# Performance work log

Hardware: AMD Instinct MI355X
Metric: run time of the kernel (lower is better)

The kernel has to match this reference:

```python
import jax, jax.numpy as jnp
import numpy as np

B, S, D = 4, 4096, 1024
DFF = 4 * D
ACTIVE = 1024  # ceil(S * 0.25)


def setup_inputs() -> dict:
    key = jax.random.key(0)
    ks = jax.random.split(key, 4)
    x = jax.random.normal(ks[0], (B, S, D), dtype=jnp.float32)
    rw = jax.random.normal(ks[1], (D,), dtype=jnp.float32) * 0.02
    rb = jnp.zeros((1,), dtype=jnp.float32)
    w1 = jax.random.normal(ks[2], (D, DFF), dtype=jnp.float32) * 0.02
    b1 = jnp.zeros((DFF,), dtype=jnp.float32)
    w2 = jax.random.normal(ks[3], (DFF, D), dtype=jnp.float32) * 0.02
    b2 = jnp.zeros((D,), dtype=jnp.float32)
    return {"x": x, "rw": rw, "rb": rb, "w1": w1, "b1": b1,
            "w2": w2, "b2": b2, "active_tokens": ACTIVE}


def reference(x, rw, rb, w1, b1, w2, b2, active_tokens):
    b, s, d = x.shape
    # router: Linear(n_embd, 1) -> [B, S] scores
    scores = jnp.einsum('bsd,d->bs', x, rw) + rb[0]
    # top-k tokens per batch row
    _, idx = jax.lax.top_k(scores, active_tokens)          # [B, K] int32
    sel = jnp.take_along_axis(x, idx[..., None], axis=1)   # [B, K, D]
    # dense MLP on selected tokens (exact GELU as in torch nn.GELU)
    h = jax.nn.gelu(jnp.einsum('bkd,df->bkf', sel, w1) + b1, approximate=False)
    out = jnp.einsum('bkf,fd->bkd', h, w2) + b2            # [B, K, D]
    # sigmoid gate from router scores of selected tokens
    gates = jax.nn.sigmoid(jnp.take_along_axis(scores, idx, axis=1))  # [B, K]
    out = out * gates[..., None]
    # scatter back into zeros at selected positions
    flat_idx = (idx + jnp.arange(b, dtype=idx.dtype)[:, None] * s).reshape(-1)
    flat_out = jnp.zeros((b * s, d), dtype=out.dtype)
    flat_out = flat_out.at[flat_idx].set(out.reshape(-1, d))
    return flat_out.reshape(b, s, d)
```

## Files before the change

kernel.cpp:

```cpp
#include <hip/hip_runtime.h>
#include <hip/hip_bf16.h>
#include <cstdint>
#include <cstddef>

#define Bz 4
#define Sz 4096
#define Dz 1024
#define DFFz 4096
#define KACT 1024

typedef __bf16 bf16;
typedef __attribute__((ext_vector_type(8))) __bf16 bf16x8;
typedef __attribute__((ext_vector_type(4))) __bf16 bf16x4;
typedef __attribute__((ext_vector_type(4))) float f32x4;

__device__ __forceinline__ void async16(const void* g, void* l) {
  __builtin_amdgcn_global_load_lds(
      (const __attribute__((address_space(1))) void*)g,
      (__attribute__((address_space(3))) void*)l, 16, 0, 0);
}

__global__ __launch_bounds__(256) void prep_k(const float* __restrict__ x,
                                              const float* __restrict__ rw,
                                              const float* __restrict__ rb,
                                              float* __restrict__ scores,
                                              float4* __restrict__ out4,
                                              const float* __restrict__ w1,
                                              bf16* __restrict__ w1T,
                                              const float* __restrict__ w2,
                                              bf16* __restrict__ w2T) {
  __shared__ float t[32][33];
  const int bid = blockIdx.x;
  const int tid = threadIdx.x;
  if (bid < 4096) {
    int row = bid * 4 + (tid >> 6);
    int lane = tid & 63;
    const float4* xr = (const float4*)(x + (size_t)row * Dz);
    const float4* wr = (const float4*)rw;
    float acc = 0.f;
#pragma unroll
    for (int i = 0; i < 4; ++i) {
      float4 a = xr[lane + i * 64];
      float4 w = wr[lane + i * 64];
      acc += a.x * w.x + a.y * w.y + a.z * w.z + a.w * w.w;
    }
#pragma unroll
    for (int d = 32; d; d >>= 1) acc += __shfl_down(acc, d, 64);
    if (lane == 0) scores[row] = acc + rb[0];
    float4* o = out4 + (size_t)bid * 4 * (Dz / 4);
    const float4 z = make_float4(0.f, 0.f, 0.f, 0.f);
#pragma unroll
    for (int i = 0; i < 4; ++i) o[tid + i * 256] = z;
  } else {
    const float* in; bf16* outp; int R, C, bx, by;
    if (bid < 8192) {
      in = w1; outp = w1T; R = Dz; C = DFFz;
      bx = (bid - 4096) & 127; by = (bid - 4096) >> 7;
    } else {
      in = w2; outp = w2T; R = DFFz; C = Dz;
      bx = (bid - 8192) & 31; by = (bid - 8192) >> 5;
    }
    int c0 = bx * 32, r0 = by * 32;
    int tx = tid & 31, ty = tid >> 5;
#pragma unroll
    for (int i = 0; i < 32; i += 8) t[ty + i][tx] = in[(size_t)(r0 + ty + i) * C + c0 + tx];
    __syncthreads();
#pragma unroll
    for (int i = 0; i < 32; i += 8)
      outp[(size_t)(c0 + ty + i) * R + r0 + tx] = (bf16)t[tx][ty + i];
  }
}

__global__ __launch_bounds__(256) void select_gather_k(
    const float* __restrict__ x, const float* __restrict__ scores,
    int* __restrict__ sel_idx, float* __restrict__ gates, bf16* __restrict__ Xsel) {
  int b = blockIdx.x >> 8;
  int s0 = (blockIdx.x & 255) * 16;
  __shared__ float sc[Sz];
  __shared__ int red[16][4];
  __shared__ int rk[16];
  const int tid = threadIdx.x;
  const int wave = tid >> 6, lane = tid & 63;
  const float* srow = scores + (size_t)b * Sz;
#pragma unroll
  for (int i = 0; i < 4; ++i)
    ((float4*)sc)[tid + i * 256] = ((const float4*)srow)[tid + i * 256];
  __syncthreads();
  float mine[16];
#pragma unroll
  for (int j = 0; j < 16; ++j) mine[j] = sc[s0 + j];
  int cnt[16] = {};
  for (int t = tid; t < Sz; t += 256) {
    float o = sc[t];
#pragma unroll
    for (int j = 0; j < 16; ++j)
      cnt[j] += (o > mine[j]) || (o == mine[j] && t < s0 + j);
  }
#pragma unroll
  for (int j = 0; j < 16; ++j) {
    int c = cnt[j];
#pragma unroll
    for (int d = 32; d; d >>= 1) c += __shfl_down(c, d, 64);
    if (lane == 0) red[j][wave] = c;
  }
  __syncthreads();
  if (tid < 16) {
    int rank = red[tid][0] + red[tid][1] + red[tid][2] + red[tid][3];
    rk[tid] = rank;
    if (rank < KACT) {
      int m = b * KACT + rank;
      sel_idx[m] = s0 + tid;
      gates[m] = 1.f / (1.f + expf(-sc[s0 + tid]));
    }
  }
  __syncthreads();
#pragma unroll
  for (int j = 0; j < 16; ++j) {
    int rank = rk[j];
    if (rank >= KACT) continue;
    int m = b * KACT + rank;
    float4 v = ((const float4*)(x + ((size_t)b * Sz + s0 + j) * Dz))[tid];
    bf16x4 o = {(bf16)v.x, (bf16)v.y, (bf16)v.z, (bf16)v.w};
    ((bf16x4*)(Xsel + (size_t)m * Dz))[tid] = o;
  }
}

#define STAGE128(k0)                                                           \
  {                                                                            \
    async16(Ag + (k0), &As[tid * 8]);                                          \
    async16(Ag + (size_t)64 * K + (k0), &As[2048 + tid * 8]);                  \
    async16(Bg + (k0), &Bs[tid * 8]);                                          \
    async16(Bg + (size_t)64 * K + (k0), &Bs[2048 + tid * 8]);                  \
  }

#define GEMM128_BODY(KV, KOFF, NITER)                                          \
  __shared__ __align__(16) bf16 As[128 * 32];                        \
  __shared__ __align__(16) bf16 Bs[128 * 32];                        \
  constexpr int K = (KV);                                                      \
  const int tid = threadIdx.x;                                                 \
  const int wave = tid >> 6, lane = tid & 63;                                  \
  const int quad = lane >> 4, l16 = lane & 15;                                 \
  const int m0 = blockIdx.y * 128, n0 = blockIdx.x * 128;                      \
  const int wm = (wave >> 1) * 64, wn = (wave & 1) * 64;                       \
    \
   \
  const bf16* Ag = A + (size_t)(m0 + (tid >> 2)) * K + (KOFF) + (tid & 3) * 8; \
  const bf16* Bg = Bt + (size_t)(n0 + (tid >> 2)) * K + (KOFF) + (tid & 3) * 8;\
  f32x4 acc[4][4] = {};                                                        \
  STAGE128(0)                                                                  \
  for (int it = 0; it < (NITER); ++it) {                                       \
    __syncthreads();                 \
    bf16x8 af[4], bfr[4];                                                      \
    _Pragma("unroll")                                                          \
    for (int i = 0; i < 4; ++i) {                                              \
      af[i] = *(const bf16x8*)&As[(wm + i * 16 + l16) * 32 + quad * 8];        \
      bfr[i] = *(const bf16x8*)&Bs[(wn + i * 16 + l16) * 32 + quad * 8];       \
    }                                                                          \
    _Pragma("unroll")                                                          \
    for (int mi = 0; mi < 4; ++mi)                                             \
      _Pragma("unroll")                                                        \
      for (int ni = 0; ni < 4; ++ni)                                           \
        acc[mi][ni] = __builtin_amdgcn_mfma_f32_16x16x32_bf16(af[mi], bfr[ni], acc[mi][ni], 0, 0, 0); \
    __syncthreads();              \
    if (it + 1 < (NITER)) { STAGE128((it + 1) * 32) }                          \
  }

__global__ __launch_bounds__(256) void gemm1_k(const bf16* __restrict__ A,
                                               const bf16* __restrict__ Bt,
                                               const float* __restrict__ bias,
                                               bf16* __restrict__ H) {
  GEMM128_BODY(Dz, 0, Dz / 32)
#pragma unroll
  for (int mi = 0; mi < 4; ++mi) {
    int mbase = m0 + wm + mi * 16 + quad * 4;
#pragma unroll
    for (int ni = 0; ni < 4; ++ni) {
      int n = n0 + wn + ni * 16 + l16;
      float bn = bias[n];
#pragma unroll
      for (int r = 0; r < 4; ++r) {
        float z = acc[mi][ni][r] + bn;
        float g = 0.5f * z * (1.f + erff(z * 0.70710678118654752f));
        H[(size_t)(mbase + r) * DFFz + n] = (bf16)g;
      }
    }
  }
}

__global__ __launch_bounds__(256) void gemm2_k(const bf16* __restrict__ A,
                                               const bf16* __restrict__ Bt,
                                               bf16* __restrict__ P) {
  GEMM128_BODY(DFFz, blockIdx.z * 2048, 2048 / 32)
  bf16* Pc = P + (size_t)blockIdx.z * Bz * KACT * Dz;
#pragma unroll
  for (int mi = 0; mi < 4; ++mi) {
    int mbase = m0 + wm + mi * 16 + quad * 4;
#pragma unroll
    for (int ni = 0; ni < 4; ++ni) {
      int n = n0 + wn + ni * 16 + l16;
#pragma unroll
      for (int r = 0; r < 4; ++r)
        Pc[(size_t)(mbase + r) * Dz + n] = (bf16)acc[mi][ni][r];
    }
  }
}

__global__ __launch_bounds__(256) void reduce_k(const bf16* __restrict__ P,
                                                const float* __restrict__ bias,
                                                const int* __restrict__ sel_idx,
                                                const float* __restrict__ gates,
                                                float* __restrict__ out) {
  int m = blockIdx.x;
  int b = m >> 10;
  int s = sel_idx[m];
  float gt = gates[m];
  int tid = threadIdx.x;
  const bf16x4* p0 = (const bf16x4*)(P + (size_t)m * Dz);
  const bf16x4* p1 = (const bf16x4*)(P + (size_t)Bz * KACT * Dz + (size_t)m * Dz);
  const float4* bv = (const float4*)bias;
  float4* orow = (float4*)(out + ((size_t)b * Sz + s) * Dz);
  bf16x4 a = p0[tid], c = p1[tid];
  float4 bb = bv[tid];
  float4 o;
  o.x = ((float)a[0] + (float)c[0] + bb.x) * gt;
  o.y = ((float)a[1] + (float)c[1] + bb.y) * gt;
  o.z = ((float)a[2] + (float)c[2] + bb.z) * gt;
  o.w = ((float)a[3] + (float)c[3] + bb.w) * gt;
  orow[tid] = o;
}

extern "C" void kernel_launch(void* const* d_in, const int* in_sizes, int n_in,
                              void* d_out, int out_size, void* d_ws, size_t ws_size,
                              hipStream_t stream) {
  (void)in_sizes; (void)n_in; (void)out_size; (void)ws_size;
  const float* x  = (const float*)d_in[0];
  const float* rw = (const float*)d_in[1];
  const float* rb = (const float*)d_in[2];
  const float* w1 = (const float*)d_in[3];
  const float* b1 = (const float*)d_in[4];
  const float* w2 = (const float*)d_in[5];
  const float* b2 = (const float*)d_in[6];
  float* out = (float*)d_out;

  char* ws = (char*)d_ws;
  float* scores = (float*)ws;  ws += (size_t)Bz * Sz * 4;
  int*   sel_idx = (int*)ws;   ws += (size_t)Bz * KACT * 4;
  float* gates = (float*)ws;   ws += (size_t)Bz * KACT * 4;
  bf16*  w2T = (bf16*)ws;      ws += (size_t)Dz * DFFz * 2;
  bf16*  H = (bf16*)ws;        ws += (size_t)Bz * KACT * DFFz * 2;
  bf16*  w1T = (bf16*)ws;      ws += (size_t)DFFz * Dz * 2;
  bf16*  Xsel = (bf16*)ws;     ws += (size_t)Bz * KACT * Dz * 2;
  bf16*  P = w1T;

  prep_k<<<3 * 4096, 256, 0, stream>>>(x, rw, rb, scores, (float4*)out, w1, w1T, w2, w2T);
  select_gather_k<<<Bz * (Sz / 16), 256, 0, stream>>>(x, scores, sel_idx, gates, Xsel);
  gemm1_k<<<dim3(DFFz / 128, (Bz * KACT) / 128), 256, 0, stream>>>(Xsel, w1T, b1, H);
  gemm2_k<<<dim3(Dz / 128, (Bz * KACT) / 128, 2), 256, 0, stream>>>(H, w2T, P);
  reduce_k<<<Bz * KACT, 256, 0, stream>>>(P, b2, sel_idx, gates, out);
}
```

Baseline: 300.9 us.

## Double-buffer GEMM tiles, swizzle blocks, fuse split-K reduce into gemm2 epilogue

Both GEMMs now use double-buffered LDS so async loads for the next K-slice are issued before the MFMAs on the current one, with one barrier per iteration instead of two. Block indices are swizzled for L2 locality, and MFMA sections are wrapped in s_setprio. Gemm2 drops split-K and uses a 128x64 tile over the full K range, writing bias-added, gated fp32 results straight into the scattered output rows. This removes the reduce kernel and the bf16 partial round-trip, at the cost of longer per-block K loops and uncoalesced-ish scatter stores from the MFMA layout.

```diff
diff --git a/kernel.cpp b/kernel.cpp
--- a/kernel.cpp
+++ b/kernel.cpp
@@ -125,51 +125,54 @@
   }
 }
 
-#define STAGE128(k0)                                                           \
-  {                                                                            \
-    async16(Ag + (k0), &As[tid * 8]);                                          \
-    async16(Ag + (size_t)64 * K + (k0), &As[2048 + tid * 8]);                  \
-    async16(Bg + (k0), &Bs[tid * 8]);                                          \
-    async16(Bg + (size_t)64 * K + (k0), &Bs[2048 + tid * 8]);                  \
-  }
-
-#define GEMM128_BODY(KV, KOFF, NITER)                                          \
-  __shared__ __align__(16) bf16 As[128 * 32];                        \
-  __shared__ __align__(16) bf16 Bs[128 * 32];                        \
-  constexpr int K = (KV);                                                      \
-  const int tid = threadIdx.x;                                                 \
-  const int wave = tid >> 6, lane = tid & 63;                                  \
-  const int quad = lane >> 4, l16 = lane & 15;                                 \
-  const int m0 = blockIdx.y * 128, n0 = blockIdx.x * 128;                      \
-  const int wm = (wave >> 1) * 64, wn = (wave & 1) * 64;                       \
-    \
-   \
-  const bf16* Ag = A + (size_t)(m0 + (tid >> 2)) * K + (KOFF) + (tid & 3) * 8; \
-  const bf16* Bg = Bt + (size_t)(n0 + (tid >> 2)) * K + (KOFF) + (tid & 3) * 8;\
-  f32x4 acc[4][4] = {};                                                        \
-  STAGE128(0)                                                                  \
-  for (int it = 0; it < (NITER); ++it) {                                       \
-    __syncthreads();                 \
-    bf16x8 af[4], bfr[4];                                                      \
-    _Pragma("unroll")                                                          \
-    for (int i = 0; i < 4; ++i) {                                              \
-      af[i] = *(const bf16x8*)&As[(wm + i * 16 + l16) * 32 + quad * 8];        \
-      bfr[i] = *(const bf16x8*)&Bs[(wn + i * 16 + l16) * 32 + quad * 8];       \
-    }                                                                          \
-    _Pragma("unroll")                                                          \
-    for (int mi = 0; mi < 4; ++mi)                                             \
-      _Pragma("unroll")                                                        \
-      for (int ni = 0; ni < 4; ++ni)                                           \
-        acc[mi][ni] = __builtin_amdgcn_mfma_f32_16x16x32_bf16(af[mi], bfr[ni], acc[mi][ni], 0, 0, 0); \
-    __syncthreads();              \
-    if (it + 1 < (NITER)) { STAGE128((it + 1) * 32) }                          \
-  }
 
 __global__ __launch_bounds__(256) void gemm1_k(const bf16* __restrict__ A,
                                                const bf16* __restrict__ Bt,
                                                const float* __restrict__ bias,
                                                bf16* __restrict__ H) {
-  GEMM128_BODY(Dz, 0, Dz / 32)
+  __shared__ __align__(16) bf16 As[2][128 * 32];
+  __shared__ __align__(16) bf16 Bs[2][128 * 32];
+  constexpr int K = Dz;
+  constexpr int NITER = Dz / 32;
+  const int tid = threadIdx.x;
+  const int wave = tid >> 6, lane = tid & 63;
+  const int quad = lane >> 4, l16 = lane & 15;
+  const int orig = blockIdx.y * 32 + blockIdx.x;
+  const int swz = ((orig & 7) << 7) | (orig >> 3);
+  const int m0 = (swz >> 5) * 128, n0 = (swz & 31) * 128;
+  const int wm = (wave >> 1) * 64, wn = (wave & 1) * 64;
+  const bf16* Ag = A + (size_t)(m0 + (tid >> 2)) * K + (tid & 3) * 8;
+  const bf16* Bg = Bt + (size_t)(n0 + (tid >> 2)) * K + (tid & 3) * 8;
+  f32x4 acc[4][4] = {};
+  async16(Ag, &As[0][tid * 8]);
+  async16(Ag + (size_t)64 * K, &As[0][2048 + tid * 8]);
+  async16(Bg, &Bs[0][tid * 8]);
+  async16(Bg + (size_t)64 * K, &Bs[0][2048 + tid * 8]);
+  __syncthreads();
+  for (int t = 0; t < NITER; ++t) {
+    const int cur = t & 1;
+    if (t + 1 < NITER) {
+      const int k0 = (t + 1) * 32;
+      async16(Ag + k0, &As[cur ^ 1][tid * 8]);
+      async16(Ag + (size_t)64 * K + k0, &As[cur ^ 1][2048 + tid * 8]);
+      async16(Bg + k0, &Bs[cur ^ 1][tid * 8]);
+      async16(Bg + (size_t)64 * K + k0, &Bs[cur ^ 1][2048 + tid * 8]);
+    }
+    bf16x8 af[4], bfr[4];
+#pragma unroll
+    for (int i = 0; i < 4; ++i) {
+      af[i] = *(const bf16x8*)&As[cur][(wm + i * 16 + l16) * 32 + quad * 8];
+      bfr[i] = *(const bf16x8*)&Bs[cur][(wn + i * 16 + l16) * 32 + quad * 8];
+    }
+    __builtin_amdgcn_s_setprio(1);
+#pragma unroll
+    for (int mi = 0; mi < 4; ++mi)
+#pragma unroll
+      for (int ni = 0; ni < 4; ++ni)
+        acc[mi][ni] = __builtin_amdgcn_mfma_f32_16x16x32_bf16(af[mi], bfr[ni], acc[mi][ni], 0, 0, 0);
+    __builtin_amdgcn_s_setprio(0);
+    __syncthreads();
+  }
 #pragma unroll
   for (int mi = 0; mi < 4; ++mi) {
     int mbase = m0 + wm + mi * 16 + quad * 4;
@@ -189,44 +192,68 @@
 
 __global__ __launch_bounds__(256) void gemm2_k(const bf16* __restrict__ A,
                                                const bf16* __restrict__ Bt,
-                                               bf16* __restrict__ P) {
-  GEMM128_BODY(DFFz, blockIdx.z * 2048, 2048 / 32)
-  bf16* Pc = P + (size_t)blockIdx.z * Bz * KACT * Dz;
+                                               const float* __restrict__ b2,
+                                               const int* __restrict__ sel_idx,
+                                               const float* __restrict__ gates,
+                                               float* __restrict__ out) {
+  __shared__ __align__(16) bf16 As[2][128 * 32];
+  __shared__ __align__(16) bf16 Bs[2][64 * 32];
+  constexpr int K = DFFz;
+  constexpr int NITER = DFFz / 32;
+  const int tid = threadIdx.x;
+  const int wave = tid >> 6, lane = tid & 63;
+  const int quad = lane >> 4, l16 = lane & 15;
+  const int orig = blockIdx.y * 16 + blockIdx.x;
+  const int swz = ((orig & 7) << 6) | (orig >> 3);
+  const int m0 = (swz >> 4) * 128, n0 = (swz & 15) * 64;
+  const int wm = (wave >> 1) * 64, wn = (wave & 1) * 32;
+  const bf16* Ag = A + (size_t)(m0 + (tid >> 2)) * K + (tid & 3) * 8;
+  const bf16* Bg = Bt + (size_t)(n0 + (tid >> 2)) * K + (tid & 3) * 8;
+  f32x4 acc[4][2] = {};
+  async16(Ag, &As[0][tid * 8]);
+  async16(Ag + (size_t)64 * K, &As[0][2048 + tid * 8]);
+  async16(Bg, &Bs[0][tid * 8]);
+  __syncthreads();
+  for (int t = 0; t < NITER; ++t) {
+    const int cur = t & 1;
+    if (t + 1 < NITER) {
+      const int k0 = (t + 1) * 32;
+      async16(Ag + k0, &As[cur ^ 1][tid * 8]);
+      async16(Ag + (size_t)64 * K + k0, &As[cur ^ 1][2048 + tid * 8]);
+      async16(Bg + k0, &Bs[cur ^ 1][tid * 8]);
+    }
+    bf16x8 af[4], bfr[2];
+#pragma unroll
+    for (int i = 0; i < 4; ++i)
+      af[i] = *(const bf16x8*)&As[cur][(wm + i * 16 + l16) * 32 + quad * 8];
+#pragma unroll
+    for (int i = 0; i < 2; ++i)
+      bfr[i] = *(const bf16x8*)&Bs[cur][(wn + i * 16 + l16) * 32 + quad * 8];
+    __builtin_amdgcn_s_setprio(1);
+#pragma unroll
+    for (int mi = 0; mi < 4; ++mi)
+#pragma unroll
+      for (int ni = 0; ni < 2; ++ni)
+        acc[mi][ni] = __builtin_amdgcn_mfma_f32_16x16x32_bf16(af[mi], bfr[ni], acc[mi][ni], 0, 0, 0);
+    __builtin_amdgcn_s_setprio(0);
+    __syncthreads();
+  }
 #pragma unroll
   for (int mi = 0; mi < 4; ++mi) {
-    int mbase = m0 + wm + mi * 16 + quad * 4;
-#pragma unroll
-    for (int ni = 0; ni < 4; ++ni) {
-      int n = n0 + wn + ni * 16 + l16;
-#pragma unroll
-      for (int r = 0; r < 4; ++r)
-        Pc[(size_t)(mbase + r) * Dz + n] = (bf16)acc[mi][ni][r];
-    }
-  }
-}
-
-__global__ __launch_bounds__(256) void reduce_k(const bf16* __restrict__ P,
-                                                const float* __restrict__ bias,
-                                                const int* __restrict__ sel_idx,
-                                                const float* __restrict__ gates,
-                                                float* __restrict__ out) {
-  int m = blockIdx.x;
-  int b = m >> 10;
-  int s = sel_idx[m];
-  float gt = gates[m];
-  int tid = threadIdx.x;
-  const bf16x4* p0 = (const bf16x4*)(P + (size_t)m * Dz);
-  const bf16x4* p1 = (const bf16x4*)(P + (size_t)Bz * KACT * Dz + (size_t)m * Dz);
-  const float4* bv = (const float4*)bias;
-  float4* orow = (float4*)(out + ((size_t)b * Sz + s) * Dz);
-  bf16x4 a = p0[tid], c = p1[tid];
-  float4 bb = bv[tid];
-  float4 o;
-  o.x = ((float)a[0] + (float)c[0] + bb.x) * gt;
-  o.y = ((float)a[1] + (float)c[1] + bb.y) * gt;
-  o.z = ((float)a[2] + (float)c[2] + bb.z) * gt;
-  o.w = ((float)a[3] + (float)c[3] + bb.w) * gt;
-  orow[tid] = o;
+#pragma unroll
+    for (int r = 0; r < 4; ++r) {
+      int m = m0 + wm + mi * 16 + quad * 4 + r;
+      int b = m >> 10;
+      int s = sel_idx[m];
+      float g = gates[m];
+      float* orow = out + ((size_t)b * Sz + s) * Dz;
+#pragma unroll
+      for (int ni = 0; ni < 2; ++ni) {
+        int n = n0 + wn + ni * 16 + l16;
+        orow[n] = (acc[mi][ni][r] + b2[n]) * g;
+      }
+    }
+  }
 }
 
 extern "C" void kernel_launch(void* const* d_in, const int* in_sizes, int n_in,
@@ -250,11 +277,9 @@
   bf16*  H = (bf16*)ws;        ws += (size_t)Bz * KACT * DFFz * 2;
   bf16*  w1T = (bf16*)ws;      ws += (size_t)DFFz * Dz * 2;
   bf16*  Xsel = (bf16*)ws;     ws += (size_t)Bz * KACT * Dz * 2;
-  bf16*  P = w1T;
 
   prep_k<<<3 * 4096, 256, 0, stream>>>(x, rw, rb, scores, (float4*)out, w1, w1T, w2, w2T);
   select_gather_k<<<Bz * (Sz / 16), 256, 0, stream>>>(x, scores, sel_idx, gates, Xsel);
   gemm1_k<<<dim3(DFFz / 128, (Bz * KACT) / 128), 256, 0, stream>>>(Xsel, w1T, b1, H);
-  gemm2_k<<<dim3(Dz / 128, (Bz * KACT) / 128, 2), 256, 0, stream>>>(H, w2T, P);
-  reduce_k<<<Bz * KACT, 256, 0, stream>>>(P, b2, sel_idx, gates, out);
-}
+  gemm2_k<<<dim3(Dz / 64, (Bz * KACT) / 128), 256, 0, stream>>>(H, w2T, b2, sel_idx, gates, out);
+}
```

After: 325.4 us. 1.08x slower.

## Triple-buffer GEMM loads with swizzled LDS, XCD-aware tile remap, fuse reduce via atomics

Applied to the files above, without the earlier changes.

Replaces the single-buffered GEMM main loop with a three-stage LDS ring and a 64-wide K step, waiting with vmcnt so global loads overlap MFMA work. LDS addresses are XOR-swizzled to avoid bank conflicts, and block IDs are remapped across XCDs. The split-K reduce kernel is removed: gemm2 adds bias, applies the gate and atomically adds fp32 results straight into the output. The output is zeroed in prep, so this saves the bf16 partial buffer and one launch, at the cost of atomic traffic and nondeterministic summation order.

```diff
diff --git a/kernel.cpp b/kernel.cpp
--- a/kernel.cpp
+++ b/kernel.cpp
@@ -125,54 +125,90 @@
   }
 }
 
-#define STAGE128(k0)                                                           \
-  {                                                                            \
-    async16(Ag + (k0), &As[tid * 8]);                                          \
-    async16(Ag + (size_t)64 * K + (k0), &As[2048 + tid * 8]);                  \
-    async16(Bg + (k0), &Bs[tid * 8]);                                          \
-    async16(Bg + (size_t)64 * K + (k0), &Bs[2048 + tid * 8]);                  \
-  }
-
-#define GEMM128_BODY(KV, KOFF, NITER)                                          \
-  __shared__ __align__(16) bf16 As[128 * 32];                        \
-  __shared__ __align__(16) bf16 Bs[128 * 32];                        \
-  constexpr int K = (KV);                                                      \
-  const int tid = threadIdx.x;                                                 \
-  const int wave = tid >> 6, lane = tid & 63;                                  \
-  const int quad = lane >> 4, l16 = lane & 15;                                 \
-  const int m0 = blockIdx.y * 128, n0 = blockIdx.x * 128;                      \
-  const int wm = (wave >> 1) * 64, wn = (wave & 1) * 64;                       \
-    \
-   \
-  const bf16* Ag = A + (size_t)(m0 + (tid >> 2)) * K + (KOFF) + (tid & 3) * 8; \
-  const bf16* Bg = Bt + (size_t)(n0 + (tid >> 2)) * K + (KOFF) + (tid & 3) * 8;\
-  f32x4 acc[4][4] = {};                                                        \
-  STAGE128(0)                                                                  \
-  for (int it = 0; it < (NITER); ++it) {                                       \
-    __syncthreads();                 \
-    bf16x8 af[4], bfr[4];                                                      \
-    _Pragma("unroll")                                                          \
-    for (int i = 0; i < 4; ++i) {                                              \
-      af[i] = *(const bf16x8*)&As[(wm + i * 16 + l16) * 32 + quad * 8];        \
-      bfr[i] = *(const bf16x8*)&Bs[(wn + i * 16 + l16) * 32 + quad * 8];       \
-    }                                                                          \
-    _Pragma("unroll")                                                          \
-    for (int mi = 0; mi < 4; ++mi)                                             \
-      _Pragma("unroll")                                                        \
-      for (int ni = 0; ni < 4; ++ni)                                           \
-        acc[mi][ni] = __builtin_amdgcn_mfma_f32_16x16x32_bf16(af[mi], bfr[ni], acc[mi][ni], 0, 0, 0); \
-    __syncthreads();              \
-    if (it + 1 < (NITER)) { STAGE128((it + 1) * 32) }                          \
-  }
+
+#define BAR_VM4 asm volatile("s_waitcnt vmcnt(4) lgkmcnt(0)\n\ts_barrier" ::: "memory")
+#define BAR_VM0 asm volatile("s_waitcnt vmcnt(0) lgkmcnt(0)\n\ts_barrier" ::: "memory")
+
+#define STG(AS, BS, T)                                                        \
+  {                                                                           \
+    size_t ko = (size_t)(T) * 64;                                             \
+    async16(pa0 + ko, (char*)AS + Ld0);                                       \
+    async16(pa1 + ko, (char*)AS + Ld1);                                       \
+    async16(pb0 + ko, (char*)BS + Ld0);                                       \
+    async16(pb1 + ko, (char*)BS + Ld1);                                       \
+  }
+
+#define GBODY(ARD, BRD, AST, BST, T, DOSTAGE, BARK)                           \
+  {                                                                           \
+    if (DOSTAGE) { STG(AST, BST, (T) + 2) }                                   \
+    bf16x8 af[4], bfr[4];                                                     \
+    const char* a_ = (const char*)ARD;                                        \
+    const char* b_ = (const char*)BRD;                                        \
+    _Pragma("unroll") for (int i = 0; i < 4; ++i) {                           \
+      af[i] = *(const bf16x8*)(a_ + aoff[i]);                                 \
+      bfr[i] = *(const bf16x8*)(b_ + boff[i]);                                \
+    }                                                                         \
+    __builtin_amdgcn_s_setprio(1);                                            \
+    _Pragma("unroll") for (int mi = 0; mi < 4; ++mi)                          \
+      _Pragma("unroll") for (int ni = 0; ni < 4; ++ni)                        \
+        acc[mi][ni] = __builtin_amdgcn_mfma_f32_16x16x32_bf16(                \
+            af[mi], bfr[ni], acc[mi][ni], 0, 0, 0);                           \
+    __builtin_amdgcn_s_setprio(0);                                            \
+    if ((BARK) == 0) { BAR_VM4; }                                             \
+    else if ((BARK) == 1) { BAR_VM0; }                                        \
+  }
+
+#define GSETUP(APTR, BPTR, KV, KOFFB)                                         \
+  const int tid = threadIdx.x;                                                \
+  const int wave = tid >> 6, lane = tid & 63;                                 \
+  const int quad = lane >> 4, l16 = lane & 15;                                \
+  const int wm = (wave >> 1) * 64, wn = (wave & 1) * 64;                      \
+  const int Ld0 = tid * 16, Ld1 = 4096 + tid * 16;                            \
+  const int q0 = Ld0 ^ (((Ld0 >> 7) & 3) << 4);                               \
+  const int q1 = Ld1 ^ (((Ld1 >> 7) & 3) << 4);                               \
+  const char* pa0 = (const char*)(APTR) +                                     \
+      ((size_t)(m0 + (q0 >> 6)) * (KV)) * 2 + (KOFFB) + (q0 & 63);            \
+  const char* pa1 = (const char*)(APTR) +                                     \
+      ((size_t)(m0 + (q1 >> 6)) * (KV)) * 2 + (KOFFB) + (q1 & 63);            \
+  const char* pb0 = (const char*)(BPTR) +                                     \
+      ((size_t)(n0 + (q0 >> 6)) * (KV)) * 2 + (KOFFB) + (q0 & 63);            \
+  const char* pb1 = (const char*)(BPTR) +                                     \
+      ((size_t)(n0 + (q1 >> 6)) * (KV)) * 2 + (KOFFB) + (q1 & 63);            \
+  int aoff[4], boff[4];                                                       \
+  _Pragma("unroll") for (int i = 0; i < 4; ++i) {                             \
+    int ra = wm + i * 16 + l16;                                               \
+    int oa = ra * 64 + quad * 16;                                             \
+    aoff[i] = oa ^ (((ra >> 1) & 3) << 4);                                    \
+    int rb = wn + i * 16 + l16;                                               \
+    int ob = rb * 64 + quad * 16;                                             \
+    boff[i] = ob ^ (((rb >> 1) & 3) << 4);                                    \
+  }                                                                           \
+  f32x4 acc[4][4] = {};
 
 __global__ __launch_bounds__(256) void gemm1_k(const bf16* __restrict__ A,
                                                const bf16* __restrict__ Bt,
                                                const float* __restrict__ bias,
                                                bf16* __restrict__ H) {
-  GEMM128_BODY(Dz, 0, Dz / 32)
+  __shared__ __align__(16) bf16 A0[4096], A1[4096], A2[4096];
+  __shared__ __align__(16) bf16 B0[4096], B1[4096], B2[4096];
+  const int orig = blockIdx.y * 32 + blockIdx.x;
+  const int wgid = (orig & 7) * 128 + (orig >> 3);
+  const int m0 = (wgid >> 5) * 128, n0 = (wgid & 31) * 128;
+  GSETUP(A, Bt, Dz, 0)
+  STG(A0, B0, 0)
+  STG(A1, B1, 1)
+  BAR_VM4;
+  for (int tt = 0; tt < 10; ++tt) {
+    const int t0 = tt * 3;
+    GBODY(A0, B0, A2, B2, t0 + 0, 1, 0)
+    GBODY(A1, B1, A0, B0, t0 + 1, 1, 0)
+    GBODY(A2, B2, A1, B1, t0 + 2, 1, 0)
+  }
+  GBODY(A0, B0, A0, B0, 30, 0, 1)
+  GBODY(A1, B1, A0, B0, 31, 0, 2)
 #pragma unroll
   for (int mi = 0; mi < 4; ++mi) {
-    int mbase = m0 + wm + mi * 16 + quad * 4;
+    int mb = m0 + wm + mi * 16 + quad * 4;
 #pragma unroll
     for (int ni = 0; ni < 4; ++ni) {
       int n = n0 + wn + ni * 16 + l16;
@@ -181,7 +217,7 @@
       for (int r = 0; r < 4; ++r) {
         float z = acc[mi][ni][r] + bn;
         float g = 0.5f * z * (1.f + erff(z * 0.70710678118654752f));
-        H[(size_t)(mbase + r) * DFFz + n] = (bf16)g;
+        H[(size_t)(mb + r) * DFFz + n] = (bf16)g;
       }
     }
   }
@@ -189,44 +225,47 @@
 
 __global__ __launch_bounds__(256) void gemm2_k(const bf16* __restrict__ A,
                                                const bf16* __restrict__ Bt,
-                                               bf16* __restrict__ P) {
-  GEMM128_BODY(DFFz, blockIdx.z * 2048, 2048 / 32)
-  bf16* Pc = P + (size_t)blockIdx.z * Bz * KACT * Dz;
+                                               const float* __restrict__ b2,
+                                               const int* __restrict__ sel_idx,
+                                               const float* __restrict__ gates,
+                                               float* __restrict__ out) {
+  __shared__ __align__(16) bf16 A0[4096], A1[4096], A2[4096];
+  __shared__ __align__(16) bf16 B0[4096], B1[4096], B2[4096];
+  const int orig = blockIdx.y * 8 + blockIdx.x;
+  const int wgid = (orig & 7) * 32 + (orig >> 3);
+  const int m0 = (wgid >> 3) * 128, n0 = (wgid & 7) * 128;
+  GSETUP(A, Bt, DFFz, (size_t)blockIdx.z * 2048 * 2)
+  STG(A0, B0, 0)
+  STG(A1, B1, 1)
+  BAR_VM4;
+  for (int tt = 0; tt < 20; ++tt) {
+    const int t0 = tt * 3;
+    GBODY(A0, B0, A2, B2, t0 + 0, 1, 0)
+    GBODY(A1, B1, A0, B0, t0 + 1, 1, 0)
+    GBODY(A2, B2, A1, B1, t0 + 2, 1, 0)
+  }
+  GBODY(A0, B0, A2, B2, 60, 1, 0)
+  GBODY(A1, B1, A0, B0, 61, 1, 0)
+  GBODY(A2, B2, A0, B0, 62, 0, 1)
+  GBODY(A0, B0, A0, B0, 63, 0, 2)
+  const bool addb = (blockIdx.z == 0);
 #pragma unroll
   for (int mi = 0; mi < 4; ++mi) {
-    int mbase = m0 + wm + mi * 16 + quad * 4;
-#pragma unroll
-    for (int ni = 0; ni < 4; ++ni) {
-      int n = n0 + wn + ni * 16 + l16;
-#pragma unroll
-      for (int r = 0; r < 4; ++r)
-        Pc[(size_t)(mbase + r) * Dz + n] = (bf16)acc[mi][ni][r];
-    }
-  }
-}
-
-__global__ __launch_bounds__(256) void reduce_k(const bf16* __restrict__ P,
-                                                const float* __restrict__ bias,
-                                                const int* __restrict__ sel_idx,
-                                                const float* __restrict__ gates,
-                                                float* __restrict__ out) {
-  int m = blockIdx.x;
-  int b = m >> 10;
-  int s = sel_idx[m];
-  float gt = gates[m];
-  int tid = threadIdx.x;
-  const bf16x4* p0 = (const bf16x4*)(P + (size_t)m * Dz);
-  const bf16x4* p1 = (const bf16x4*)(P + (size_t)Bz * KACT * Dz + (size_t)m * Dz);
-  const float4* bv = (const float4*)bias;
-  float4* orow = (float4*)(out + ((size_t)b * Sz + s) * Dz);
-  bf16x4 a = p0[tid], c = p1[tid];
-  float4 bb = bv[tid];
-  float4 o;
-  o.x = ((float)a[0] + (float)c[0] + bb.x) * gt;
-  o.y = ((float)a[1] + (float)c[1] + bb.y) * gt;
-  o.z = ((float)a[2] + (float)c[2] + bb.z) * gt;
-  o.w = ((float)a[3] + (float)c[3] + bb.w) * gt;
-  orow[tid] = o;
+#pragma unroll
+    for (int r = 0; r < 4; ++r) {
+      int m = m0 + wm + mi * 16 + quad * 4 + r;
+      int b = m >> 10;
+      int s = sel_idx[m];
+      float g = gates[m];
+      float* orow = out + ((size_t)b * Sz + s) * Dz;
+#pragma unroll
+      for (int ni = 0; ni < 4; ++ni) {
+        int n = n0 + wn + ni * 16 + l16;
+        float v = acc[mi][ni][r] + (addb ? b2[n] : 0.f);
+        atomicAdd(&orow[n], v * g);
+      }
+    }
+  }
 }
 
 extern "C" void kernel_launch(void* const* d_in, const int* in_sizes, int n_in,
@@ -250,11 +289,9 @@
   bf16*  H = (bf16*)ws;        ws += (size_t)Bz * KACT * DFFz * 2;
   bf16*  w1T = (bf16*)ws;      ws += (size_t)DFFz * Dz * 2;
   bf16*  Xsel = (bf16*)ws;     ws += (size_t)Bz * KACT * Dz * 2;
-  bf16*  P = w1T;
 
   prep_k<<<3 * 4096, 256, 0, stream>>>(x, rw, rb, scores, (float4*)out, w1, w1T, w2, w2T);
   select_gather_k<<<Bz * (Sz / 16), 256, 0, stream>>>(x, scores, sel_idx, gates, Xsel);
-  gemm1_k<<<dim3(DFFz / 128, (Bz * KACT) / 128), 256, 0, stream>>>(Xsel, w1T, b1, H);
-  gemm2_k<<<dim3(Dz / 128, (Bz * KACT) / 128, 2), 256, 0, stream>>>(H, w2T, P);
-  reduce_k<<<Bz * KACT, 256, 0, stream>>>(P, b2, sel_idx, gates, out);
-}
+  gemm1_k<<<dim3(32, 32), 256, 0, stream>>>(Xsel, w1T, b1, H);
+  gemm2_k<<<dim3(8, 32, 2), 256, 0, stream>>>(H, w2T, b2, sel_idx, gates, out);
+}
```

Measured after the change: 306.4 us. Within noise of the previous version (+1.8%).
